# Optimization experiments

Measured on AMD Instinct MI355X. Metric: run time of the kernel, lower is better.

The kernel has to match this reference:

```python
import jax, jax.numpy as jnp
import numpy as np

# Sizes
N, T, P, D = 1000, 4, 10, 13          # nodes, point types, edge types (T*(T+1)/2), basis dim per point
F, H, EA, K, E = 128, 128, 16, 64, 20000  # node feat, edge hidden, edge attr/feat, edge op bottleneck, edges
I_NODE = D * (D + 1) // 2             # 91: symmetric ('ij=ji') self-block irreps dim
I_EDGE = D * D                        # 169: generic ('ij') block irreps dim
AVG_NEIGH = 20.0


def setup_inputs() -> dict:
    ks = jax.random.split(jax.random.key(0), 16)
    Fin = H + 2 * F                   # edge-op input: [edge_msg, node_h_i, node_h_j]
    return {
        'node_feats': jax.random.normal(ks[0], (N, F), jnp.float32),
        'node_attrs': jax.random.uniform(ks[1], (N, T), dtype=jnp.float32),
        'edge_feats': jax.random.normal(ks[2], (E, EA), jnp.float32),
        'edge_attrs': jax.random.normal(ks[3], (E, EA), jnp.float32),
        'edge_index': jax.random.randint(ks[4], (2, E), 0, N),
        'node_types': jax.random.randint(ks[5], (N,), 0, T),
        'edge_types': jax.random.randint(ks[6], (E,), 0, P),
        'W_msg': jax.random.normal(ks[7], (F, F), jnp.float32) / np.float32(np.sqrt(F)),
        'W_attr': jax.random.normal(ks[8], (T, F), jnp.float32) / np.float32(np.sqrt(T)),
        'W_em': jax.random.normal(ks[9], (2 * F + 2 * EA, H), jnp.float32) / np.float32(np.sqrt(2 * F + 2 * EA)),
        'W_proj': jax.random.normal(ks[10], (Fin, K), jnp.float32) / np.float32(np.sqrt(Fin)),
        'W_node': jax.random.normal(ks[11], (T, F, I_NODE), jnp.float32) / np.float32(np.sqrt(F)),
        'W_edge': jax.random.normal(ks[12], (P, K, I_EDGE), jnp.float32) / np.float32(np.sqrt(K)),
        'cob_node': jax.random.normal(ks[13], (T, I_NODE, D, D), jnp.float32) / np.float32(D),
        'cob_edge': jax.random.normal(ks[14], (P, I_EDGE, D, D), jnp.float32) / np.float32(D),
    }


def reference(node_feats, node_attrs, edge_feats, edge_attrs, edge_index, node_types,
              edge_types, W_msg, W_attr, W_em, W_proj, W_node, W_edge, cob_node, cob_edge):
    src, dst = edge_index[0], edge_index[1]
    # --- node message passing (NodeMessageBlock, simplified linear-aggregate form) ---
    m = node_feats @ W_msg                                             # [N, F]
    agg = jax.ops.segment_sum(m[src], dst, num_segments=N) \
        + jax.ops.segment_sum(m[dst], src, num_segments=N)             # symmetric edge list: both dirs
    node_h = node_feats + agg / AVG_NEIGH + node_attrs @ W_attr        # [N, F]
    # --- edge messages (EdgeMessageBlock, simplified) ---
    e_in = jnp.concatenate([node_h[src], node_h[dst], edge_feats, edge_attrs], axis=-1)
    edge_msg = jnp.tanh(e_in @ W_em)                                   # [E, H]
    # --- self-interaction blocks: per-type gather -> op -> einsum('ni,ixy->nxy', ., cob) ---
    node_irred = jnp.einsum('nf,nfi->ni', node_h, W_node[node_types])  # [N, I_NODE]
    node_blocks = jnp.einsum('ni,nixy->nxy', node_irred, cob_node[node_types])  # [N, D, D]
    # --- interaction blocks: per-edge-type op + change of basis, transpose-symmetrized ---
    onehot = jax.nn.one_hot(edge_types, P, dtype=node_feats.dtype)     # [E, P] type selector

    def edge_block(a, b):
        h = jnp.concatenate([edge_msg, a, b], axis=-1) @ W_proj        # [E, K]
        irr = jnp.einsum('epi,ep->ei', jnp.einsum('ek,pki->epi', h, W_edge), onehot)  # [E, I_EDGE]
        return jnp.einsum('epxy,ep->exy', jnp.einsum('ei,pixy->epxy', irr, cob_edge), onehot)  # [E, D, D]

    blk_ij = edge_block(node_h[src], node_h[dst])
    blk_ji = edge_block(node_h[dst], node_h[src])
    edge_blocks = 0.5 * (blk_ij + jnp.swapaxes(blk_ji, -1, -2))        # symm_transpose
    # --- scatter blocks into the dense symmetric block matrix ---
    off = jnp.arange(D)
    nidx = jnp.arange(N)[:, None] * D + off                            # [N, D] diagonal block rows/cols
    rs = src[:, None] * D + off                                        # [E, D]
    cs = dst[:, None] * D + off
    M = jnp.zeros((N * D, N * D), node_feats.dtype)
    M = M.at[nidx[:, :, None], nidx[:, None, :]].add(node_blocks)
    M = M.at[rs[:, :, None], cs[:, None, :]].add(edge_blocks)
    M = M.at[cs[:, :, None], rs[:, None, :]].add(jnp.swapaxes(edge_blocks, -1, -2))
    return M
```

## Files before the change

kernel.cpp:

```cpp
#include <hip/hip_runtime.h>
#include <cmath>

#define NN   1000
#define TT   4
#define PP   10
#define DD   13
#define FF   128
#define HH   128
#define EAA  16
#define KDIM 64
#define EE   20000
#define I_NODE 91
#define I_EDGE 169
#define MROW  13000

__global__ __launch_bounds__(128) void k_node_msg(
    const float* __restrict__ nf, const float* __restrict__ Wmsg,
    float* __restrict__ m, float* __restrict__ agg) {
  int n = blockIdx.x, j = threadIdx.x;
  __shared__ float row[FF];
  row[j] = nf[n * FF + j];
  __syncthreads();
  float acc = 0.f;
#pragma unroll 8
  for (int f = 0; f < FF; ++f) acc += row[f] * Wmsg[f * FF + j];
  m[n * FF + j] = acc;
  agg[n * FF + j] = 0.f;
}

__global__ __launch_bounds__(256) void k_scatter(
    const float* __restrict__ m, const int* __restrict__ src,
    const int* __restrict__ dst, float* __restrict__ agg) {
  int idx = blockIdx.x * 256 + threadIdx.x;
  if (idx >= EE * FF) return;
  int e = idx >> 7, j = idx & 127;
  int s = src[e], d = dst[e];
  atomicAdd(&agg[d * FF + j], m[s * FF + j]);
  atomicAdd(&agg[s * FF + j], m[d * FF + j]);
}

__global__ __launch_bounds__(128) void k_node_h(
    const float* __restrict__ nf, const float* __restrict__ agg,
    const float* __restrict__ na, const float* __restrict__ Wattr,
    float* __restrict__ nh) {
  int n = blockIdx.x, j = threadIdx.x;
  float a = 0.f;
#pragma unroll
  for (int t = 0; t < TT; ++t) a += na[n * TT + t] * Wattr[t * FF + j];
  nh[n * FF + j] = nf[n * FF + j] + agg[n * FF + j] * (1.0f / 20.0f) + a;
}

#define EPB 8
__global__ __launch_bounds__(128) void k_edge_msg(
    const float* __restrict__ nh, const float* __restrict__ ef,
    const float* __restrict__ ea, const int* __restrict__ src,
    const int* __restrict__ dst, const float* __restrict__ Wem,
    float* __restrict__ emsg) {
  int e0 = blockIdx.x * EPB;
  int j = threadIdx.x;
  __shared__ float xin[EPB][2 * FF + 2 * EAA];
  for (int e = 0; e < EPB; ++e) {
    int ee = e0 + e;
    int s = src[ee], d = dst[ee];
    for (int i = j; i < 288; i += 128) {
      float v;
      if (i < 128)      v = nh[s * FF + i];
      else if (i < 256) v = nh[d * FF + (i - 128)];
      else if (i < 272) v = ef[ee * EAA + (i - 256)];
      else              v = ea[ee * EAA + (i - 272)];
      xin[e][i] = v;
    }
  }
  __syncthreads();
  float acc[EPB];
#pragma unroll
  for (int e = 0; e < EPB; ++e) acc[e] = 0.f;
  for (int i = 0; i < 288; ++i) {
    float w = Wem[i * HH + j];
#pragma unroll
    for (int e = 0; e < EPB; ++e) acc[e] += xin[e][i] * w;
  }
#pragma unroll
  for (int e = 0; e < EPB; ++e) emsg[(e0 + e) * HH + j] = tanhf(acc[e]);
}

__global__ __launch_bounds__(256) void k_node_block(
    const float* __restrict__ nh, const int* __restrict__ ntype,
    const float* __restrict__ Wnode, const float* __restrict__ cob,
    float* __restrict__ M) {
  int n = blockIdx.x, t = threadIdx.x;
  int ty = ntype[n];
  __shared__ float row[FF];
  __shared__ float irr[I_NODE];
  if (t < FF) row[t] = nh[n * FF + t];
  __syncthreads();
  if (t < I_NODE) {
    float acc = 0.f;
    const float* W = Wnode + ty * FF * I_NODE + t;
#pragma unroll 4
    for (int f = 0; f < FF; ++f) acc += row[f] * W[f * I_NODE];
    irr[t] = acc;
  }
  __syncthreads();
  if (t < I_EDGE) {
    float acc = 0.f;
    const float* C = cob + ty * I_NODE * I_EDGE + t;
    for (int i = 0; i < I_NODE; ++i) acc += irr[i] * C[i * I_EDGE];
    int x = t / DD, y = t % DD;
    atomicAdd(&M[(size_t)(n * DD + x) * MROW + (n * DD + y)], acc);
  }
}

__global__ __launch_bounds__(256) void k_edge_block(
    const float* __restrict__ nh, const float* __restrict__ emsg,
    const int* __restrict__ src, const int* __restrict__ dst,
    const int* __restrict__ etype, const float* __restrict__ Wproj,
    const float* __restrict__ Wedge, const float* __restrict__ cob,
    float* __restrict__ M) {
  int e = blockIdx.x, t = threadIdx.x;
  int s = src[e], d = dst[e], p = etype[e];
  __shared__ float xin[384];
  __shared__ float hpij[256], hpji[256];
  __shared__ float h_ij[KDIM], h_ji[KDIM];
  __shared__ float irr_ij[I_EDGE], irr_ji[I_EDGE];
  __shared__ float blk_ij[I_EDGE], blk_ji[I_EDGE];

  if (t < 128) {
    xin[t] = emsg[e * HH + t];
    xin[256 + t] = nh[d * FF + t];
  } else {
    xin[t] = nh[s * FF + (t - 128)];
  }
  __syncthreads();

  {
    int k = t & 63, seg = t >> 6;
    float aij = 0.f, aji = 0.f;
    const float* Wp = Wproj + k;
    int i0 = seg * 96;
    for (int i = i0; i < i0 + 96; ++i) {
      float w = Wp[i * KDIM];
      int iswap = (i < 128) ? i : ((i < 256) ? i + 128 : i - 128);
      aij += xin[i] * w;
      aji += xin[iswap] * w;
    }
    hpij[t] = aij; hpji[t] = aji;
  }
  __syncthreads();
  if (t < KDIM) {
    h_ij[t] = hpij[t] + hpij[t + 64] + hpij[t + 128] + hpij[t + 192];
    h_ji[t] = hpji[t] + hpji[t + 64] + hpji[t + 128] + hpji[t + 192];
  }
  __syncthreads();

  if (t < I_EDGE) {
    float aij = 0.f, aji = 0.f;
    const float* W = Wedge + p * KDIM * I_EDGE + t;
#pragma unroll 4
    for (int k = 0; k < KDIM; ++k) {
      float w = W[k * I_EDGE];
      aij += h_ij[k] * w;
      aji += h_ji[k] * w;
    }
    irr_ij[t] = aij; irr_ji[t] = aji;
  }
  __syncthreads();

  if (t < I_EDGE) {
    float aij = 0.f, aji = 0.f;
    const float* C = cob + p * I_EDGE * I_EDGE + t;
    for (int i = 0; i < I_EDGE; ++i) {
      float c = C[i * I_EDGE];
      aij += irr_ij[i] * c;
      aji += irr_ji[i] * c;
    }
    blk_ij[t] = aij; blk_ji[t] = aji;
  }
  __syncthreads();

  if (t < I_EDGE) {
    int x = t / DD, y = t % DD;
    float eb = 0.5f * (blk_ij[t] + blk_ji[y * DD + x]);
    atomicAdd(&M[(size_t)(s * DD + x) * MROW + (d * DD + y)], eb);
    atomicAdd(&M[(size_t)(d * DD + y) * MROW + (s * DD + x)], eb);
  }
}

extern "C" void kernel_launch(void* const* d_in, const int* in_sizes, int n_in,
                              void* d_out, int out_size, void* d_ws, size_t ws_size,
                              hipStream_t stream) {
  const float* node_feats = (const float*)d_in[0];
  const float* node_attrs = (const float*)d_in[1];
  const float* edge_feats = (const float*)d_in[2];
  const float* edge_attrs = (const float*)d_in[3];
  const int*   edge_index = (const int*)d_in[4];
  const int*   node_types = (const int*)d_in[5];
  const int*   edge_types = (const int*)d_in[6];
  const float* W_msg  = (const float*)d_in[7];
  const float* W_attr = (const float*)d_in[8];
  const float* W_em   = (const float*)d_in[9];
  const float* W_proj = (const float*)d_in[10];
  const float* W_node = (const float*)d_in[11];
  const float* W_edge = (const float*)d_in[12];
  const float* cob_node = (const float*)d_in[13];
  const float* cob_edge = (const float*)d_in[14];

  float* M  = (float*)d_out;
  float* ws = (float*)d_ws;
  float* m_buf = ws;
  float* agg   = ws + 128000;
  float* nh    = ws + 256000;
  float* emsg  = ws + 384000;

  const int* src = edge_index;
  const int* dst = edge_index + EE;

  hipMemsetAsync(d_out, 0, (size_t)out_size * sizeof(float), stream);

  k_node_msg <<<NN, 128, 0, stream>>>(node_feats, W_msg, m_buf, agg);
  k_scatter  <<<(EE * FF) / 256, 256, 0, stream>>>(m_buf, src, dst, agg);
  k_node_h   <<<NN, 128, 0, stream>>>(node_feats, agg, node_attrs, W_attr, nh);
  k_edge_msg <<<EE / EPB, 128, 0, stream>>>(nh, edge_feats, edge_attrs, src, dst, W_em, emsg);
  k_node_block<<<NN, 256, 0, stream>>>(nh, node_types, W_node, cob_node, M);
  k_edge_block<<<EE, 256, 0, stream>>>(nh, emsg, src, dst, edge_types,
                                       W_proj, W_edge, cob_edge, M);
}
```

Measured before the change: 1.029 ms.

## Bucket edges by type and process eight same-type edges per block

Edges are grouped by edge type with an atomic counting pass. The edge-block kernel then handles 8 edges of one type per workgroup, so each W_proj, W_edge and cob_edge load is reused across 16 ij/ji vectors instead of 2. This targets the per-edge reloading of the 169x169 change-of-basis and weight matrices. The memset is replaced by a float4 zero kernel. The grid launches many blocks that exit immediately, and the order of atomic adds now depends on bucketing.

```diff
diff --git a/kernel.cpp b/kernel.cpp
--- a/kernel.cpp
+++ b/kernel.cpp
@@ -13,6 +13,16 @@
 #define I_NODE 91
 #define I_EDGE 169
 #define MROW  13000
+#define EB   8
+#define NI   (2*EB)
+#define CHUNKS_PER_TYPE ((EE + EB - 1) / EB)
+
+__global__ __launch_bounds__(256) void k_zero(float4* __restrict__ p, long n4) {
+  long i = (long)blockIdx.x * 256 + threadIdx.x;
+  long stride = (long)gridDim.x * 256;
+  float4 z = make_float4(0.f, 0.f, 0.f, 0.f);
+  for (; i < n4; i += stride) p[i] = z;
+}
 
 __global__ __launch_bounds__(128) void k_node_msg(
     const float* __restrict__ nf, const float* __restrict__ Wmsg,
@@ -111,78 +121,118 @@
   }
 }
 
+__global__ void k_zero_counts(int* __restrict__ cnt) {
+  if (threadIdx.x < PP) cnt[threadIdx.x] = 0;
+}
+
+__global__ __launch_bounds__(256) void k_bucket(
+    const int* __restrict__ etype, int* __restrict__ cnt, int* __restrict__ list) {
+  int e = blockIdx.x * 256 + threadIdx.x;
+  if (e >= EE) return;
+  int p = etype[e];
+  int r = atomicAdd(&cnt[p], 1);
+  list[p * EE + r] = e;
+}
+
 __global__ __launch_bounds__(256) void k_edge_block(
     const float* __restrict__ nh, const float* __restrict__ emsg,
     const int* __restrict__ src, const int* __restrict__ dst,
-    const int* __restrict__ etype, const float* __restrict__ Wproj,
-    const float* __restrict__ Wedge, const float* __restrict__ cob,
-    float* __restrict__ M) {
-  int e = blockIdx.x, t = threadIdx.x;
-  int s = src[e], d = dst[e], p = etype[e];
-  __shared__ float xin[384];
-  __shared__ float hpij[256], hpji[256];
-  __shared__ float h_ij[KDIM], h_ji[KDIM];
-  __shared__ float irr_ij[I_EDGE], irr_ji[I_EDGE];
-  __shared__ float blk_ij[I_EDGE], blk_ji[I_EDGE];
-
-  if (t < 128) {
-    xin[t] = emsg[e * HH + t];
-    xin[256 + t] = nh[d * FF + t];
-  } else {
-    xin[t] = nh[s * FF + (t - 128)];
+    const int* __restrict__ cnt, const int* __restrict__ list,
+    const float* __restrict__ Wproj, const float* __restrict__ Wedge,
+    const float* __restrict__ cob, float* __restrict__ M) {
+  int p = blockIdx.x / CHUNKS_PER_TYPE;
+  int chunk = blockIdx.x % CHUNKS_PER_TYPE;
+  int ecnt = cnt[p];
+  int base = chunk * EB;
+  if (base >= ecnt) return;
+  int nval = ecnt - base; if (nval > EB) nval = EB;
+
+  int t = threadIdx.x;
+  __shared__ float xin[EB][384];
+  __shared__ float sh_h[NI][KDIM];
+  __shared__ float sh_irr[NI][I_EDGE];
+  __shared__ float sh_blk[NI][I_EDGE];
+  __shared__ int se[EB], de[EB], eid[EB];
+
+  if (t < EB) {
+    int slot = (t < nval) ? t : 0;
+    int e = list[p * EE + base + slot];
+    eid[t] = e; se[t] = src[e]; de[t] = dst[e];
+  }
+  __syncthreads();
+
+  for (int e = 0; e < EB; ++e) {
+    int ee = eid[e], s = se[e], d = de[e];
+    for (int i = t; i < 384; i += 256) {
+      float v;
+      if (i < 128)      v = emsg[ee * HH + i];
+      else if (i < 256) v = nh[s * FF + (i - 128)];
+      else              v = nh[d * FF + (i - 256)];
+      xin[e][i] = v;
+    }
   }
   __syncthreads();
 
   {
-    int k = t & 63, seg = t >> 6;
-    float aij = 0.f, aji = 0.f;
+    int k = t & 63, g = t >> 6;
+    int e0 = g * 2, e1 = g * 2 + 1;
+    float a0 = 0.f, a1 = 0.f, a2 = 0.f, a3 = 0.f;
     const float* Wp = Wproj + k;
-    int i0 = seg * 96;
-    for (int i = i0; i < i0 + 96; ++i) {
+    for (int i = 0; i < 384; ++i) {
       float w = Wp[i * KDIM];
       int iswap = (i < 128) ? i : ((i < 256) ? i + 128 : i - 128);
-      aij += xin[i] * w;
-      aji += xin[iswap] * w;
-    }
-    hpij[t] = aij; hpji[t] = aji;
-  }
-  __syncthreads();
-  if (t < KDIM) {
-    h_ij[t] = hpij[t] + hpij[t + 64] + hpij[t + 128] + hpij[t + 192];
-    h_ji[t] = hpji[t] + hpji[t + 64] + hpji[t + 128] + hpji[t + 192];
-  }
-  __syncthreads();
-
-  if (t < I_EDGE) {
-    float aij = 0.f, aji = 0.f;
+      a0 += xin[e0][i] * w;
+      a1 += xin[e0][iswap] * w;
+      a2 += xin[e1][i] * w;
+      a3 += xin[e1][iswap] * w;
+    }
+    sh_h[e0 * 2 + 0][k] = a0;
+    sh_h[e0 * 2 + 1][k] = a1;
+    sh_h[e1 * 2 + 0][k] = a2;
+    sh_h[e1 * 2 + 1][k] = a3;
+  }
+  __syncthreads();
+
+  if (t < I_EDGE) {
+    float acc[NI];
+#pragma unroll
+    for (int q = 0; q < NI; ++q) acc[q] = 0.f;
     const float* W = Wedge + p * KDIM * I_EDGE + t;
-#pragma unroll 4
+#pragma unroll 2
     for (int k = 0; k < KDIM; ++k) {
       float w = W[k * I_EDGE];
-      aij += h_ij[k] * w;
-      aji += h_ji[k] * w;
-    }
-    irr_ij[t] = aij; irr_ji[t] = aji;
-  }
-  __syncthreads();
-
-  if (t < I_EDGE) {
-    float aij = 0.f, aji = 0.f;
+#pragma unroll
+      for (int q = 0; q < NI; ++q) acc[q] += sh_h[q][k] * w;
+    }
+#pragma unroll
+    for (int q = 0; q < NI; ++q) sh_irr[q][t] = acc[q];
+  }
+  __syncthreads();
+
+  if (t < I_EDGE) {
+    float acc[NI];
+#pragma unroll
+    for (int q = 0; q < NI; ++q) acc[q] = 0.f;
     const float* C = cob + p * I_EDGE * I_EDGE + t;
+#pragma unroll 2
     for (int i = 0; i < I_EDGE; ++i) {
       float c = C[i * I_EDGE];
-      aij += irr_ij[i] * c;
-      aji += irr_ji[i] * c;
-    }
-    blk_ij[t] = aij; blk_ji[t] = aji;
+#pragma unroll
+      for (int q = 0; q < NI; ++q) acc[q] += sh_irr[q][i] * c;
+    }
+#pragma unroll
+    for (int q = 0; q < NI; ++q) sh_blk[q][t] = acc[q];
   }
   __syncthreads();
 
   if (t < I_EDGE) {
     int x = t / DD, y = t % DD;
-    float eb = 0.5f * (blk_ij[t] + blk_ji[y * DD + x]);
-    atomicAdd(&M[(size_t)(s * DD + x) * MROW + (d * DD + y)], eb);
-    atomicAdd(&M[(size_t)(d * DD + y) * MROW + (s * DD + x)], eb);
+    for (int e = 0; e < nval; ++e) {
+      int s = se[e], d = de[e];
+      float eb = 0.5f * (sh_blk[e * 2 + 0][t] + sh_blk[e * 2 + 1][y * DD + x]);
+      atomicAdd(&M[(size_t)(s * DD + x) * MROW + (d * DD + y)], eb);
+      atomicAdd(&M[(size_t)(d * DD + y) * MROW + (s * DD + x)], eb);
+    }
   }
 }
 
@@ -211,17 +261,21 @@
   float* agg   = ws + 128000;
   float* nh    = ws + 256000;
   float* emsg  = ws + 384000;
+  int*   cnt   = (int*)(ws + 2944000);
+  int*   list  = cnt + 16;
 
   const int* src = edge_index;
   const int* dst = edge_index + EE;
 
-  hipMemsetAsync(d_out, 0, (size_t)out_size * sizeof(float), stream);
-
-  k_node_msg <<<NN, 128, 0, stream>>>(node_feats, W_msg, m_buf, agg);
-  k_scatter  <<<(EE * FF) / 256, 256, 0, stream>>>(m_buf, src, dst, agg);
-  k_node_h   <<<NN, 128, 0, stream>>>(node_feats, agg, node_attrs, W_attr, nh);
-  k_edge_msg <<<EE / EPB, 128, 0, stream>>>(nh, edge_feats, edge_attrs, src, dst, W_em, emsg);
-  k_node_block<<<NN, 256, 0, stream>>>(nh, node_types, W_node, cob_node, M);
-  k_edge_block<<<EE, 256, 0, stream>>>(nh, emsg, src, dst, edge_types,
-                                       W_proj, W_edge, cob_edge, M);
-}
+  long n4 = (long)out_size / 4;
+  k_zero       <<<16384, 256, 0, stream>>>((float4*)M, n4);
+  k_zero_counts<<<1, 64, 0, stream>>>(cnt);
+  k_bucket     <<<(EE + 255) / 256, 256, 0, stream>>>(edge_types, cnt, list);
+  k_node_msg   <<<NN, 128, 0, stream>>>(node_feats, W_msg, m_buf, agg);
+  k_scatter    <<<(EE * FF) / 256, 256, 0, stream>>>(m_buf, src, dst, agg);
+  k_node_h     <<<NN, 128, 0, stream>>>(node_feats, agg, node_attrs, W_attr, nh);
+  k_edge_msg   <<<EE / EPB, 128, 0, stream>>>(nh, edge_feats, edge_attrs, src, dst, W_em, emsg);
+  k_node_block <<<NN, 256, 0, stream>>>(nh, node_types, W_node, cob_node, M);
+  k_edge_block <<<PP * CHUNKS_PER_TYPE, 256, 0, stream>>>(
+      nh, emsg, src, dst, cnt, list, W_proj, W_edge, cob_edge, M);
+}
```

Result: slower. 1.253 ms (+21.7%).

## Precombine edge/node weight with change-of-basis and batch two edges per block

Applied to the files above, without the earlier changes.

Per call, W_edge is precomputed against cob_edge and W_node against cob_node, giving combined weights that each node and edge block applies in one matvec. This removes the 169x169 per-edge change-of-basis product, the largest per-edge cost. The edge kernel now handles two edges per block so the projection and combined weights are shared, and inner loops read float4 from LDS. The memset becomes a float4 zero kernel. Precombining changes floating-point summation order and adds two small setup kernels plus workspace.

```diff
diff --git a/kernel.cpp b/kernel.cpp
--- a/kernel.cpp
+++ b/kernel.cpp
@@ -13,6 +13,39 @@
 #define I_NODE 91
 #define I_EDGE 169
 #define MROW  13000
+
+__global__ __launch_bounds__(256) void k_zero(float4* __restrict__ p, long n4) {
+  long i = (long)blockIdx.x * 256 + threadIdx.x;
+  if (i < n4) p[i] = make_float4(0.f, 0.f, 0.f, 0.f);
+}
+
+__global__ __launch_bounds__(192) void k_comb_edge(
+    const float* __restrict__ We, const float* __restrict__ cob,
+    float* __restrict__ Wcomb) {
+  int pk = blockIdx.x;
+  int p = pk >> 6;
+  int t = threadIdx.x;
+  if (t >= I_EDGE) return;
+  float acc = 0.f;
+  const float* wrow = We + pk * I_EDGE;
+  const float* crow = cob + p * I_EDGE * I_EDGE + t;
+  for (int i = 0; i < I_EDGE; ++i) acc += wrow[i] * crow[i * I_EDGE];
+  Wcomb[pk * I_EDGE + t] = acc;
+}
+
+__global__ __launch_bounds__(192) void k_comb_node(
+    const float* __restrict__ Wn, const float* __restrict__ cob,
+    float* __restrict__ Wnc) {
+  int tf = blockIdx.x;
+  int ty = tf >> 7;
+  int t = threadIdx.x;
+  if (t >= I_EDGE) return;
+  float acc = 0.f;
+  const float* wrow = Wn + tf * I_NODE;
+  const float* crow = cob + ty * I_NODE * I_EDGE + t;
+  for (int i = 0; i < I_NODE; ++i) acc += wrow[i] * crow[i * I_EDGE];
+  Wnc[tf * I_EDGE + t] = acc;
+}
 
 __global__ __launch_bounds__(128) void k_node_msg(
     const float* __restrict__ nf, const float* __restrict__ Wmsg,
@@ -75,114 +108,137 @@
   float acc[EPB];
 #pragma unroll
   for (int e = 0; e < EPB; ++e) acc[e] = 0.f;
-  for (int i = 0; i < 288; ++i) {
-    float w = Wem[i * HH + j];
-#pragma unroll
-    for (int e = 0; e < EPB; ++e) acc[e] += xin[e][i] * w;
+  for (int c = 0; c < 288; c += 4) {
+    float4 xv[EPB];
+#pragma unroll
+    for (int e = 0; e < EPB; ++e) xv[e] = *(const float4*)&xin[e][c];
+#pragma unroll
+    for (int sub = 0; sub < 4; ++sub) {
+      float w = Wem[(c + sub) * HH + j];
+      const float* xs;
+#pragma unroll
+      for (int e = 0; e < EPB; ++e) {
+        float x = (sub == 0) ? xv[e].x : (sub == 1) ? xv[e].y : (sub == 2) ? xv[e].z : xv[e].w;
+        acc[e] += x * w;
+      }
+    }
   }
 #pragma unroll
   for (int e = 0; e < EPB; ++e) emsg[(e0 + e) * HH + j] = tanhf(acc[e]);
 }
 
-__global__ __launch_bounds__(256) void k_node_block(
+__global__ __launch_bounds__(192) void k_node_block(
     const float* __restrict__ nh, const int* __restrict__ ntype,
-    const float* __restrict__ Wnode, const float* __restrict__ cob,
-    float* __restrict__ M) {
+    const float* __restrict__ Wnc, float* __restrict__ M) {
   int n = blockIdx.x, t = threadIdx.x;
   int ty = ntype[n];
   __shared__ float row[FF];
-  __shared__ float irr[I_NODE];
   if (t < FF) row[t] = nh[n * FF + t];
-  __syncthreads();
-  if (t < I_NODE) {
-    float acc = 0.f;
-    const float* W = Wnode + ty * FF * I_NODE + t;
-#pragma unroll 4
-    for (int f = 0; f < FF; ++f) acc += row[f] * W[f * I_NODE];
-    irr[t] = acc;
-  }
   __syncthreads();
   if (t < I_EDGE) {
     float acc = 0.f;
-    const float* C = cob + ty * I_NODE * I_EDGE + t;
-    for (int i = 0; i < I_NODE; ++i) acc += irr[i] * C[i * I_EDGE];
+    const float* W = Wnc + ty * FF * I_EDGE + t;
+#pragma unroll 4
+    for (int f = 0; f < FF; ++f) acc += row[f] * W[f * I_EDGE];
     int x = t / DD, y = t % DD;
     atomicAdd(&M[(size_t)(n * DD + x) * MROW + (n * DD + y)], acc);
   }
 }
 
-__global__ __launch_bounds__(256) void k_edge_block(
+#define E2 2
+__global__ __launch_bounds__(256) void k_edge_blk(
     const float* __restrict__ nh, const float* __restrict__ emsg,
     const int* __restrict__ src, const int* __restrict__ dst,
     const int* __restrict__ etype, const float* __restrict__ Wproj,
-    const float* __restrict__ Wedge, const float* __restrict__ cob,
-    float* __restrict__ M) {
-  int e = blockIdx.x, t = threadIdx.x;
-  int s = src[e], d = dst[e], p = etype[e];
-  __shared__ float xin[384];
-  __shared__ float hpij[256], hpji[256];
-  __shared__ float h_ij[KDIM], h_ji[KDIM];
-  __shared__ float irr_ij[I_EDGE], irr_ji[I_EDGE];
-  __shared__ float blk_ij[I_EDGE], blk_ji[I_EDGE];
-
-  if (t < 128) {
-    xin[t] = emsg[e * HH + t];
-    xin[256 + t] = nh[d * FF + t];
-  } else {
-    xin[t] = nh[s * FF + (t - 128)];
+    const float* __restrict__ Wcomb, float* __restrict__ M) {
+  int e0 = blockIdx.x * E2;
+  int t = threadIdx.x;
+  __shared__ float xin[E2][384];
+  __shared__ float hp[4][256];
+  __shared__ float hv[4][KDIM];
+  __shared__ float tji[E2][I_EDGE];
+  __shared__ int se[E2], de[E2], pe[E2];
+
+  if (t < E2) {
+    int e = e0 + t;
+    se[t] = src[e]; de[t] = dst[e]; pe[t] = etype[e];
+  }
+  __syncthreads();
+  for (int e = 0; e < E2; ++e) {
+    int ee = e0 + e, s = se[e], d = de[e];
+    if (t < 128) {
+      xin[e][t] = emsg[ee * HH + t];
+      xin[e][256 + t] = nh[d * FF + t];
+    } else {
+      xin[e][t] = nh[s * FF + (t - 128)];
+    }
   }
   __syncthreads();
 
   {
     int k = t & 63, seg = t >> 6;
-    float aij = 0.f, aji = 0.f;
+    float a0 = 0.f, a1 = 0.f, a2 = 0.f, a3 = 0.f;
     const float* Wp = Wproj + k;
     int i0 = seg * 96;
-    for (int i = i0; i < i0 + 96; ++i) {
-      float w = Wp[i * KDIM];
-      int iswap = (i < 128) ? i : ((i < 256) ? i + 128 : i - 128);
-      aij += xin[i] * w;
-      aji += xin[iswap] * w;
-    }
-    hpij[t] = aij; hpji[t] = aji;
+    for (int c = i0; c < i0 + 96; c += 4) {
+      int cs = (c < 128) ? c : (c < 256 ? c + 128 : c - 128);
+      float4 x0 = *(const float4*)&xin[0][c];
+      float4 x0s = *(const float4*)&xin[0][cs];
+      float4 x1 = *(const float4*)&xin[1][c];
+      float4 x1s = *(const float4*)&xin[1][cs];
+      float w0 = Wp[(c + 0) * KDIM], w1 = Wp[(c + 1) * KDIM];
+      float w2 = Wp[(c + 2) * KDIM], w3 = Wp[(c + 3) * KDIM];
+      a0 += x0.x * w0 + x0.y * w1 + x0.z * w2 + x0.w * w3;
+      a1 += x0s.x * w0 + x0s.y * w1 + x0s.z * w2 + x0s.w * w3;
+      a2 += x1.x * w0 + x1.y * w1 + x1.z * w2 + x1.w * w3;
+      a3 += x1s.x * w0 + x1s.y * w1 + x1s.z * w2 + x1s.w * w3;
+    }
+    hp[0][t] = a0; hp[1][t] = a1; hp[2][t] = a2; hp[3][t] = a3;
   }
   __syncthreads();
   if (t < KDIM) {
-    h_ij[t] = hpij[t] + hpij[t + 64] + hpij[t + 128] + hpij[t + 192];
-    h_ji[t] = hpji[t] + hpji[t + 64] + hpji[t + 128] + hpji[t + 192];
-  }
-  __syncthreads();
-
+#pragma unroll
+    for (int q = 0; q < 4; ++q)
+      hv[q][t] = hp[q][t] + hp[q][t + 64] + hp[q][t + 128] + hp[q][t + 192];
+  }
+  __syncthreads();
+
+  float b0 = 0.f, b1 = 0.f, b2 = 0.f, b3 = 0.f;
   if (t < I_EDGE) {
-    float aij = 0.f, aji = 0.f;
-    const float* W = Wedge + p * KDIM * I_EDGE + t;
-#pragma unroll 4
-    for (int k = 0; k < KDIM; ++k) {
-      float w = W[k * I_EDGE];
-      aij += h_ij[k] * w;
-      aji += h_ji[k] * w;
-    }
-    irr_ij[t] = aij; irr_ji[t] = aji;
-  }
-  __syncthreads();
-
-  if (t < I_EDGE) {
-    float aij = 0.f, aji = 0.f;
-    const float* C = cob + p * I_EDGE * I_EDGE + t;
-    for (int i = 0; i < I_EDGE; ++i) {
-      float c = C[i * I_EDGE];
-      aij += irr_ij[i] * c;
-      aji += irr_ji[i] * c;
-    }
-    blk_ij[t] = aij; blk_ji[t] = aji;
+    const float* W0 = Wcomb + pe[0] * KDIM * I_EDGE + t;
+    const float* W1 = Wcomb + pe[1] * KDIM * I_EDGE + t;
+    for (int k = 0; k < KDIM; k += 4) {
+      float4 h0 = *(const float4*)&hv[0][k];
+      float4 h1 = *(const float4*)&hv[1][k];
+      float4 h2 = *(const float4*)&hv[2][k];
+      float4 h3 = *(const float4*)&hv[3][k];
+      float u0 = W0[(k + 0) * I_EDGE], u1 = W0[(k + 1) * I_EDGE];
+      float u2 = W0[(k + 2) * I_EDGE], u3 = W0[(k + 3) * I_EDGE];
+      float v0 = W1[(k + 0) * I_EDGE], v1 = W1[(k + 1) * I_EDGE];
+      float v2 = W1[(k + 2) * I_EDGE], v3 = W1[(k + 3) * I_EDGE];
+      b0 += h0.x * u0 + h0.y * u1 + h0.z * u2 + h0.w * u3;
+      b1 += h1.x * u0 + h1.y * u1 + h1.z * u2 + h1.w * u3;
+      b2 += h2.x * v0 + h2.y * v1 + h2.z * v2 + h2.w * v3;
+      b3 += h3.x * v0 + h3.y * v1 + h3.z * v2 + h3.w * v3;
+    }
+    tji[0][t] = b1; tji[1][t] = b3;
   }
   __syncthreads();
 
   if (t < I_EDGE) {
     int x = t / DD, y = t % DD;
-    float eb = 0.5f * (blk_ij[t] + blk_ji[y * DD + x]);
-    atomicAdd(&M[(size_t)(s * DD + x) * MROW + (d * DD + y)], eb);
-    atomicAdd(&M[(size_t)(d * DD + y) * MROW + (s * DD + x)], eb);
+    {
+      int s = se[0], d = de[0];
+      float eb = 0.5f * (b0 + tji[0][y * DD + x]);
+      atomicAdd(&M[(size_t)(s * DD + x) * MROW + (d * DD + y)], eb);
+      atomicAdd(&M[(size_t)(d * DD + y) * MROW + (s * DD + x)], eb);
+    }
+    {
+      int s = se[1], d = de[1];
+      float eb = 0.5f * (b2 + tji[1][y * DD + x]);
+      atomicAdd(&M[(size_t)(s * DD + x) * MROW + (d * DD + y)], eb);
+      atomicAdd(&M[(size_t)(d * DD + y) * MROW + (s * DD + x)], eb);
+    }
   }
 }
 
@@ -211,17 +267,21 @@
   float* agg   = ws + 128000;
   float* nh    = ws + 256000;
   float* emsg  = ws + 384000;
+  float* Wcomb = ws + 2944000;
+  float* Wnc   = ws + 3052160;
 
   const int* src = edge_index;
   const int* dst = edge_index + EE;
 
-  hipMemsetAsync(d_out, 0, (size_t)out_size * sizeof(float), stream);
-
-  k_node_msg <<<NN, 128, 0, stream>>>(node_feats, W_msg, m_buf, agg);
-  k_scatter  <<<(EE * FF) / 256, 256, 0, stream>>>(m_buf, src, dst, agg);
-  k_node_h   <<<NN, 128, 0, stream>>>(node_feats, agg, node_attrs, W_attr, nh);
-  k_edge_msg <<<EE / EPB, 128, 0, stream>>>(nh, edge_feats, edge_attrs, src, dst, W_em, emsg);
-  k_node_block<<<NN, 256, 0, stream>>>(nh, node_types, W_node, cob_node, M);
-  k_edge_block<<<EE, 256, 0, stream>>>(nh, emsg, src, dst, edge_types,
-                                       W_proj, W_edge, cob_edge, M);
-}
+  long n4 = (long)out_size / 4;
+  k_zero      <<<(int)((n4 + 255) / 256), 256, 0, stream>>>((float4*)M, n4);
+  k_comb_edge <<<PP * KDIM, 192, 0, stream>>>(W_edge, cob_edge, Wcomb);
+  k_comb_node <<<TT * FF, 192, 0, stream>>>(W_node, cob_node, Wnc);
+  k_node_msg  <<<NN, 128, 0, stream>>>(node_feats, W_msg, m_buf, agg);
+  k_scatter   <<<(EE * FF) / 256, 256, 0, stream>>>(m_buf, src, dst, agg);
+  k_node_h    <<<NN, 128, 0, stream>>>(node_feats, agg, node_attrs, W_attr, nh);
+  k_edge_msg  <<<EE / EPB, 128, 0, stream>>>(nh, edge_feats, edge_attrs, src, dst, W_em, emsg);
+  k_node_block<<<NN, 192, 0, stream>>>(nh, node_types, Wnc, M);
+  k_edge_blk  <<<EE / E2, 256, 0, stream>>>(nh, emsg, src, dst, edge_types,
+                                            W_proj, Wcomb, M);
+}
```

Result: faster. 919.9 us (-10.6%).
